# Optimization experiments

Measured on AMD Instinct MI355X. Metric: run time of the kernel, lower is better.

The kernel has to match this reference:

```python
import jax, jax.numpy as jnp
import numpy as np

NOISE_EPS = 0.01
TOP_K = 2
EXPERT_NUM = 16


def setup_inputs() -> dict:
    key = jax.random.key(0)
    ks = jax.random.split(key, 9)
    B, C, H, W, E = 64, 768, 64, 64, EXPERT_NUM
    return {
        "x": jax.random.normal(ks[0], (B, C, H, W), jnp.float32),
        "m": jax.random.normal(ks[1], (B, 1, H, W), jnp.float32),
        "z": jax.random.normal(ks[2], (B, E), jnp.float32),
        "conv_w": jax.random.normal(ks[3], (1, 1, 1, 1), jnp.float32) * 0.1,
        "conv_b": jax.random.normal(ks[4], (1,), jnp.float32) * 0.1,
        "wg": jax.random.normal(ks[5], (E, C), jnp.float32) * 0.02,
        "bg": jax.random.normal(ks[6], (E,), jnp.float32) * 0.02,
        "wn": jax.random.normal(ks[7], (E, C), jnp.float32) * 0.02,
        "bn": jax.random.normal(ks[8], (E,), jnp.float32) * 0.02,
    }


def reference(x, m, z, conv_w, conv_b, wg, bg, wn, bn):
    # 1x1 conv with 1 in/out channel == scalar affine on the noise map
    noise_map = m * conv_w[0, 0, 0, 0] + conv_b[0]          # [B,1,H,W]
    x = x + noise_map * x                                    # [B,C,H,W]
    pooled = jnp.mean(x, axis=(2, 3))                        # global avg pool -> [B,C]
    clean_logits = pooled @ wg.T + bg                        # [B,E]
    noise_stddev = jax.nn.softplus(pooled @ wn.T + bn) + NOISE_EPS
    logits = clean_logits + z * noise_stddev                 # train=True path
    k1 = min(TOP_K + 1, EXPERT_NUM)
    top_logits, top_indices = jax.lax.top_k(logits, k1)
    top_k_logits = top_logits[:, :TOP_K]
    top_k_indices = top_indices[:, :TOP_K]
    top_k_gates = jax.nn.softmax(top_k_logits, axis=1)
    B = logits.shape[0]
    gates = jnp.zeros_like(logits).at[jnp.arange(B)[:, None], top_k_indices].set(top_k_gates)
    load = gates.sum(axis=0)                                 # [E]
    return gates, load
```

## Files before the change

### kernel.cpp

```cpp
#include <hip/hip_runtime.h>
#include <hip/hip_bf16.h>
#include <math.h>

#define B_ 64
#define C_ 768
#define HW_ 4096
#define E_ 16
#define NOISE_EPS_ 0.01f

__global__ __launch_bounds__(256) void pool_kernel(
    const float* __restrict__ x, const float* __restrict__ m,
    const float* __restrict__ conv_w, const float* __restrict__ conv_b,
    float* __restrict__ pooled)
{
    const int bc = blockIdx.x;
    const int b  = bc / C_;
    const int t  = threadIdx.x;

    const float4* xp = (const float4*)(x + (size_t)bc * HW_);
    const float4* mp = (const float4*)(m + (size_t)b  * HW_);

    const float cw = conv_w[0];
    const float w0 = 1.0f + conv_b[0];

    float sum = 0.0f;
#pragma unroll
    for (int k = 0; k < 4; ++k) {
        const float4 xv = xp[t + k * 256];
        const float4 mv = mp[t + k * 256];
        sum += xv.x * fmaf(mv.x, cw, w0);
        sum += xv.y * fmaf(mv.y, cw, w0);
        sum += xv.z * fmaf(mv.z, cw, w0);
        sum += xv.w * fmaf(mv.w, cw, w0);
    }

#pragma unroll
    for (int off = 32; off > 0; off >>= 1)
        sum += __shfl_down(sum, off, 64);

    __shared__ float red[4];
    if ((t & 63) == 0) red[t >> 6] = sum;
    __syncthreads();
    if (t == 0)
        pooled[bc] = (red[0] + red[1] + red[2] + red[3]) * (1.0f / (float)HW_);
}

__global__ __launch_bounds__(256) void gate_kernel(
    const float* __restrict__ pooled, const float* __restrict__ z,
    const float* __restrict__ wg, const float* __restrict__ bg,
    const float* __restrict__ wn, const float* __restrict__ bn,
    float* __restrict__ out)
{
    const int b = blockIdx.x;
    const int t = threadIdx.x;

    __shared__ float sp[C_];
    __shared__ float lg[E_];

    for (int i = t; i < C_; i += 256) sp[i] = pooled[b * C_ + i];
    __syncthreads();

    const int e = t >> 4;
    const int j = t & 15;

    float pg = 0.0f, pn = 0.0f;
    for (int c = j; c < C_; c += 16) {
        const float p = sp[c];
        pg = fmaf(p, wg[e * C_ + c], pg);
        pn = fmaf(p, wn[e * C_ + c], pn);
    }
#pragma unroll
    for (int off = 8; off > 0; off >>= 1) {
        pg += __shfl_down(pg, off, 16);
        pn += __shfl_down(pn, off, 16);
    }
    if (j == 0) {
        const float clean = pg + bg[e];
        const float npre  = pn + bn[e];
        const float splus = fmaxf(npre, 0.0f) + log1pf(expf(-fabsf(npre)));
        lg[e] = clean + z[b * E_ + e] * (splus + NOISE_EPS_);
    }
    __syncthreads();

    if (t == 0) {
        float l0 = -INFINITY, l1 = -INFINITY;
        int   i0 = 0,         i1 = 0;
#pragma unroll
        for (int k = 0; k < E_; ++k) {
            const float v = lg[k];
            if (v > l0)      { l1 = l0; i1 = i0; l0 = v; i0 = k; }
            else if (v > l1) { l1 = v;  i1 = k; }
        }
        const float g0 = 1.0f / (1.0f + expf(l1 - l0));
        const float g1 = 1.0f - g0;
        float* row = out + b * E_;
#pragma unroll
        for (int k = 0; k < E_; ++k)
            row[k] = (k == i0) ? g0 : ((k == i1) ? g1 : 0.0f);
    }
}

__global__ void load_kernel(const float* __restrict__ gates, float* __restrict__ load)
{
    const int e = threadIdx.x;
    if (e < E_) {
        float s = 0.0f;
        for (int b = 0; b < B_; ++b) s += gates[b * E_ + e];
        load[e] = s;
    }
}

extern "C" void kernel_launch(void* const* d_in, const int* in_sizes, int n_in,
                              void* d_out, int out_size, void* d_ws, size_t ws_size,
                              hipStream_t stream)
{
    const float* x      = (const float*)d_in[0];
    const float* m      = (const float*)d_in[1];
    const float* z      = (const float*)d_in[2];
    const float* conv_w = (const float*)d_in[3];
    const float* conv_b = (const float*)d_in[4];
    const float* wg     = (const float*)d_in[5];
    const float* bg     = (const float*)d_in[6];
    const float* wn     = (const float*)d_in[7];
    const float* bn     = (const float*)d_in[8];

    float* out    = (float*)d_out;
    float* pooled = (float*)d_ws;

    pool_kernel<<<B_ * C_, 256, 0, stream>>>(x, m, conv_w, conv_b, pooled);
    gate_kernel<<<B_, 256, 0, stream>>>(pooled, z, wg, bg, wn, bn, out);
    load_kernel<<<1, 64, 0, stream>>>(out, out + B_ * E_);
}
```

Baseline: 1.006 ms.

## Process 16 channel rows per pool block, reusing noise-map weights

```diff
diff --git a/kernel.cpp b/kernel.cpp
--- a/kernel.cpp
+++ b/kernel.cpp
@@ -8,41 +8,71 @@
 #define E_ 16
 #define NOISE_EPS_ 0.01f
 
+#define ROWS_ 16
+
+typedef float f32x4 __attribute__((ext_vector_type(4)));
+
 __global__ __launch_bounds__(256) void pool_kernel(
     const float* __restrict__ x, const float* __restrict__ m,
     const float* __restrict__ conv_w, const float* __restrict__ conv_b,
     float* __restrict__ pooled)
 {
-    const int bc = blockIdx.x;
-    const int b  = bc / C_;
-    const int t  = threadIdx.x;
-
-    const float4* xp = (const float4*)(x + (size_t)bc * HW_);
-    const float4* mp = (const float4*)(m + (size_t)b  * HW_);
+    const int g    = blockIdx.x;
+    const int row0 = g * ROWS_;
+    const int b    = row0 / C_;
+    const int t    = threadIdx.x;
 
     const float cw = conv_w[0];
     const float w0 = 1.0f + conv_b[0];
 
-    float sum = 0.0f;
+    const f32x4* mp = (const f32x4*)(m + (size_t)b * HW_);
+    f32x4 wv[4];
 #pragma unroll
     for (int k = 0; k < 4; ++k) {
-        const float4 xv = xp[t + k * 256];
-        const float4 mv = mp[t + k * 256];
-        sum += xv.x * fmaf(mv.x, cw, w0);
-        sum += xv.y * fmaf(mv.y, cw, w0);
-        sum += xv.z * fmaf(mv.z, cw, w0);
-        sum += xv.w * fmaf(mv.w, cw, w0);
+        const f32x4 mv = mp[t + k * 256];
+        wv[k].x = fmaf(mv.x, cw, w0);
+        wv[k].y = fmaf(mv.y, cw, w0);
+        wv[k].z = fmaf(mv.z, cw, w0);
+        wv[k].w = fmaf(mv.w, cw, w0);
+    }
+
+    const f32x4* xp = (const f32x4*)(x + (size_t)row0 * HW_);
+    float rsum[ROWS_];
+#pragma unroll
+    for (int r = 0; r < ROWS_; ++r) rsum[r] = 0.0f;
+
+#pragma unroll
+    for (int r = 0; r < ROWS_; ++r) {
+        float s = 0.0f;
+#pragma unroll
+        for (int k = 0; k < 4; ++k) {
+            const f32x4 xv = __builtin_nontemporal_load(xp + (size_t)r * 1024 + t + k * 256);
+            s += xv.x * wv[k].x;
+            s += xv.y * wv[k].y;
+            s += xv.z * wv[k].z;
+            s += xv.w * wv[k].w;
+        }
+        rsum[r] = s;
     }
 
 #pragma unroll
-    for (int off = 32; off > 0; off >>= 1)
-        sum += __shfl_down(sum, off, 64);
+    for (int off = 32; off > 0; off >>= 1) {
+#pragma unroll
+        for (int r = 0; r < ROWS_; ++r)
+            rsum[r] += __shfl_down(rsum[r], off, 64);
+    }
 
-    __shared__ float red[4];
-    if ((t & 63) == 0) red[t >> 6] = sum;
+    __shared__ float red[4][ROWS_];
+    const int wid  = t >> 6;
+    const int lane = t & 63;
+    if (lane == 0) {
+#pragma unroll
+        for (int r = 0; r < ROWS_; ++r) red[wid][r] = rsum[r];
+    }
     __syncthreads();
-    if (t == 0)
-        pooled[bc] = (red[0] + red[1] + red[2] + red[3]) * (1.0f / (float)HW_);
+    if (t < ROWS_)
+        pooled[row0 + t] =
+            (red[0][t] + red[1][t] + red[2][t] + red[3][t]) * (1.0f / (float)HW_);
 }
 
 __global__ __launch_bounds__(256) void gate_kernel(
@@ -127,7 +157,7 @@
     float* out    = (float*)d_out;
     float* pooled = (float*)d_ws;
 
-    pool_kernel<<<B_ * C_, 256, 0, stream>>>(x, m, conv_w, conv_b, pooled);
+    pool_kernel<<<(B_ * C_) / ROWS_, 256, 0, stream>>>(x, m, conv_w, conv_b, pooled);
     gate_kernel<<<B_, 256, 0, stream>>>(pooled, z, wg, bg, wn, bn, out);
     load_kernel<<<1, 64, 0, stream>>>(out, out + B_ * E_);
 }
```

After: 997.3 us. Within noise of the previous version (-0.8%).
